# Performance work log

Measured on AMD Instinct MI355X. Metric: run time of the kernel, lower is better.

## Reference

```python
import jax, jax.numpy as jnp
import numpy as np
import math

B, SQ, SK = 8, 1024, 1024
DIM_Q = DIM_K = DIM_V = 512
H = 8
EPS = 1e-5
INF = jnp.float32(1e38)


def _ln(x, g, b):
    mu = jnp.mean(x, axis=-1, keepdims=True)
    var = jnp.mean(jnp.square(x - mu), axis=-1, keepdims=True)
    return (x - mu) * jax.lax.rsqrt(var + EPS) * g + b


def setup_inputs() -> dict:
    key = jax.random.key(0)
    ks = jax.random.split(key, 12)
    s = 1.0 / math.sqrt(DIM_V)
    return {
        "queries": jax.random.normal(ks[0], (B, SQ, DIM_Q), jnp.float32),
        "keys": jax.random.normal(ks[1], (B, SK, DIM_K), jnp.float32),
        # binary presence masks (as in the original usage)
        "presence_q": (jax.random.uniform(ks[2], (B, SQ)) > 0.1).astype(jnp.float32),
        "presence_k": (jax.random.uniform(ks[3], (B, SK)) > 0.1).astype(jnp.float32),
        "num_heads": H,
        "Wq": jax.random.normal(ks[4], (DIM_Q, DIM_V), jnp.float32) * s,
        "bq": jnp.zeros((DIM_V,), jnp.float32),
        "Wk": jax.random.normal(ks[5], (DIM_K, DIM_V), jnp.float32) * s,
        "bk": jnp.zeros((DIM_V,), jnp.float32),
        "Wv": jax.random.normal(ks[6], (DIM_K, DIM_V), jnp.float32) * s,
        "bv": jnp.zeros((DIM_V,), jnp.float32),
        "Wo": jax.random.normal(ks[7], (DIM_V, DIM_V), jnp.float32) * s,
        "bo": jnp.zeros((DIM_V,), jnp.float32),
        "g0": jnp.ones((DIM_V,), jnp.float32),
        "b0": jnp.zeros((DIM_V,), jnp.float32),
        "g1": jnp.ones((DIM_V,), jnp.float32),
        "b1": jnp.zeros((DIM_V,), jnp.float32),
    }


def reference(queries, keys, presence_q, presence_k, num_heads,
              Wq, bq, Wk, bk, Wv, bv, Wo, bo, g0, b0, g1, b1):
    b, sq, _ = queries.shape
    dim_v = Wq.shape[1]
    d = dim_v // num_heads
    q = queries @ Wq + bq                              # [B,Sq,V]
    k = keys @ Wk + bk                                 # [B,Sk,V]
    v = keys @ Wv + bv                                 # [B,Sk,V]
    qh = q.reshape(b, sq, num_heads, d)
    kh = k.reshape(b, -1, num_heads, d)
    vh = v.reshape(b, -1, num_heads, d)
    logits = jnp.einsum('bqhd,bkhd->bhqk', qh, kh) / jnp.float32(math.sqrt(dim_v))
    pq = presence_q[:, None, :, None]                  # [B,1,Sq,1]
    logits = pq * logits - (1.0 - pq) * INF
    pk = presence_k[:, None, None, :]                  # [B,1,1,Sk]
    logits = pk * logits - (1.0 - pk) * INF
    A = jax.nn.softmax(logits, axis=-1)                # [B,H,Sq,Sk]
    o = qh + jnp.einsum('bhqk,bkhd->bqhd', A, vh)      # residual add of Q_
    o = o.reshape(b, sq, dim_v)
    o = _ln(o, g0, b0)
    o = o + jax.nn.relu(o @ Wo + bo)
    o = _ln(o, g1, b1)
    return o
```

## Files before the change

### kernel.cpp

```cpp
#include <hip/hip_runtime.h>

typedef __attribute__((ext_vector_type(8))) short short8;
typedef __attribute__((ext_vector_type(4))) float f32x4;

#define SCALE2 0.06375871571f

__device__ __forceinline__ float bfu(unsigned short u){
  return __uint_as_float(((unsigned int)u) << 16);
}
__device__ __forceinline__ unsigned short f2b(float x){
  unsigned int b = __float_as_uint(x);
  return (unsigned short)((b + 0x7fffu + ((b>>16)&1u)) >> 16);
}
__device__ __forceinline__ uint4 pack8(const float* f){
  float4 a = *(const float4*)f, b = *(const float4*)(f+4);
  uint4 r;
  r.x = (unsigned)f2b(a.x) | ((unsigned)f2b(a.y)<<16);
  r.y = (unsigned)f2b(a.z) | ((unsigned)f2b(a.w)<<16);
  r.z = (unsigned)f2b(b.x) | ((unsigned)f2b(b.y)<<16);
  r.w = (unsigned)f2b(b.z) | ((unsigned)f2b(b.w)<<16);
  return r;
}

__global__ __launch_bounds__(256) void prep_inputs(
    const float* Wq, const float* Wk, const float* Wv, const float* Wo,
    const float* q, const float* k, unsigned short* wt, unsigned short* qk_dst)
{
  const int id = blockIdx.x, t = threadIdx.x;
  if (id < 256){
    const int m = id >> 6;
    const float* W = (m==0)?Wq:(m==1)?Wk:(m==2)?Wv:Wo;
    unsigned short* dst = wt + (long)m*262144;
    __shared__ unsigned short tile[64][72];
    const int n0 = ((id>>3)&7)*64, k0 = (id&7)*64;
    {
      int r = t>>2, c0 = (t&3)*16;
      uint4 u0 = pack8(W + (long)(k0+r)*512 + n0 + c0);
      uint4 u1 = pack8(W + (long)(k0+r)*512 + n0 + c0 + 8);
      unsigned short* us0 = (unsigned short*)&u0;
      unsigned short* us1 = (unsigned short*)&u1;
      #pragma unroll
      for (int i=0;i<8;++i) tile[c0+i][r] = us0[i];
      #pragma unroll
      for (int i=0;i<8;++i) tile[c0+8+i][r] = us1[i];
    }
    __syncthreads();
    {
      int n = t>>2, ks = (t&3)*16;
      *(uint4*)(dst + (long)(n0+n)*512 + k0 + ks)     = *(uint4*)&tile[n][ks];
      *(uint4*)(dst + (long)(n0+n)*512 + k0 + ks + 8) = *(uint4*)&tile[n][ks+8];
    }
  } else {
    long i = ((long)(id-256)*256 + t)*8;
    const float* src = (i < 4194304) ? q + i : k + (i - 4194304);
    *(uint4*)(qk_dst + i) = pack8(src);
  }
}

__global__ __launch_bounds__(256) void proj_mfma(
    const unsigned short* qin, const unsigned short* kin, const unsigned short* wt,
    const float* bq, const float* bk, const float* bv,
    unsigned short* q_bf, unsigned short* k_bf, unsigned short* vt_bf)
{
  const int mat = blockIdx.z;
  const unsigned short* A = (mat==0)? qin : kin;
  const unsigned short* Wt = wt + (long)mat*262144;
  const float* bias = (mat==0)?bq:(mat==1)?bk:bv;
  const int row0 = blockIdx.y*128, col0 = blockIdx.x*128;
  __shared__ unsigned short As[2][128][40];
  __shared__ unsigned short Ws[2][128][40];
  const int t = threadIdx.x;
  const int lane = t & 63, wid = t >> 6;
  const int ln = lane & 15, quad = lane >> 4;
  const int wy = wid >> 1, wx = wid & 1;
  f32x4 acc[4][4];
  #pragma unroll
  for (int i=0;i<4;++i){
    #pragma unroll
    for (int j=0;j<4;++j) acc[i][j] = (f32x4){0.f,0.f,0.f,0.f};
  }
  const int sr = t>>1, sk0 = (t&1)*16;
  const unsigned short* Arow = A  + (long)(row0+sr)*512 + sk0;
  const unsigned short* Wrow = Wt + (long)(col0+sr)*512 + sk0;
  uint4 a0 = *(const uint4*)(Arow);
  uint4 a1 = *(const uint4*)(Arow + 8);
  uint4 w0 = *(const uint4*)(Wrow);
  uint4 w1 = *(const uint4*)(Wrow + 8);
  *(uint4*)&As[0][sr][sk0]   = a0;
  *(uint4*)&As[0][sr][sk0+8] = a1;
  *(uint4*)&Ws[0][sr][sk0]   = w0;
  *(uint4*)&Ws[0][sr][sk0+8] = w1;
  __syncthreads();
  for (int it=0; it<16; ++it){
    const int cur = it & 1;
    if (it < 15){
      a0 = *(const uint4*)(Arow + (it+1)*32);
      a1 = *(const uint4*)(Arow + (it+1)*32 + 8);
      w0 = *(const uint4*)(Wrow + (it+1)*32);
      w1 = *(const uint4*)(Wrow + (it+1)*32 + 8);
    }
    short8 a[4], b[4];
    #pragma unroll
    for (int mt=0;mt<4;++mt) a[mt] = *(const short8*)&As[cur][wy*64+mt*16+ln][quad*8];
    #pragma unroll
    for (int nt=0;nt<4;++nt) b[nt] = *(const short8*)&Ws[cur][wx*64+nt*16+ln][quad*8];
    #pragma unroll
    for (int mt=0;mt<4;++mt){
      #pragma unroll
      for (int nt=0;nt<4;++nt)
        acc[mt][nt] = __builtin_amdgcn_mfma_f32_16x16x32_bf16(a[mt], b[nt], acc[mt][nt], 0,0,0);
    }
    if (it < 15){
      *(uint4*)&As[cur^1][sr][sk0]   = a0;
      *(uint4*)&As[cur^1][sr][sk0+8] = a1;
      *(uint4*)&Ws[cur^1][sr][sk0]   = w0;
      *(uint4*)&Ws[cur^1][sr][sk0+8] = w1;
    }
    __syncthreads();
  }
  float bias_v[4];
  #pragma unroll
  for (int nt=0;nt<4;++nt) bias_v[nt] = bias[col0 + wx*64 + nt*16 + ln];
  if (mat < 2){
    unsigned short* dst = (mat==0)? q_bf : k_bf;
    #pragma unroll
    for (int mt=0;mt<4;++mt){
      int row = row0 + wy*64 + mt*16 + quad*4;
      #pragma unroll
      for (int nt=0;nt<4;++nt){
        int col = col0 + wx*64 + nt*16 + ln;
        #pragma unroll
        for (int r=0;r<4;++r)
          dst[(long)(row+r)*512 + col] = f2b(acc[mt][nt][r] + bias_v[nt]);
      }
    }
  } else {
    #pragma unroll
    for (int mt=0;mt<4;++mt){
      int row = row0 + wy*64 + mt*16 + quad*4;
      int bb = row >> 10, sk = row & 1023;
      #pragma unroll
      for (int nt=0;nt<4;++nt){
        int col = col0 + wx*64 + nt*16 + ln;
        int h = col >> 6, dd = col & 63;
        uint2 pk2; unsigned short* pp = (unsigned short*)&pk2;
        #pragma unroll
        for (int r=0;r<4;++r) pp[r] = f2b(acc[mt][nt][r] + bias_v[nt]);
        *(uint2*)(vt_bf + (((long)((bb*8+h)*64+dd)) << 10) + sk) = pk2;
      }
    }
  }
}

__global__ __launch_bounds__(256, 2) void attn_mfma(
    const unsigned short* q_bf, const unsigned short* k_bf, const unsigned short* vt_bf,
    const float* pres_q, const float* pres_k, unsigned short* o_bf)
{
  const int bx = blockIdx.x;
  const int b = bx >> 3, h = bx & 7;
  const int q0 = blockIdx.y * 128;
  const int t = threadIdx.x;
  const int lane = t & 63, wid = t >> 6, ln = lane & 15, quad = lane >> 4;
  __shared__ unsigned short Pw[4][32][72];

  const unsigned short* Kb  = k_bf  + ((long)b*1024)*512 + h*64;
  const unsigned short* Vb  = vt_bf + (((long)(b*8+h)) << 16);
  const float* pkb = pres_k + b*1024;

  short8 aq[2][2];
  float av[2], mval[2];
  #pragma unroll
  for (int st=0;st<2;++st){
    int qi = q0 + wid*32 + st*16 + ln;
    const unsigned short* qrow = q_bf + ((long)(b*1024 + qi))*512 + h*64;
    aq[st][0] = *(const short8*)(qrow + quad*8);
    aq[st][1] = *(const short8*)(qrow + 32 + quad*8);
    av[st]   = SCALE2 * pres_q[b*1024 + qi];
    mval[st] = (av[st] == 0.f) ? 0.f : -43.f;
  }
  f32x4 oacc[2][4];
  #pragma unroll
  for (int st=0;st<2;++st){
    #pragma unroll
    for (int i=0;i<4;++i) oacc[st][i] = (f32x4){0.f,0.f,0.f,0.f};
  }
  float lsum[2] = {0.f, 0.f};

  short8 kf0[4], kf1[4];
  #pragma unroll
  for (int kt=0;kt<4;++kt){
    const unsigned short* kp = Kb + ((long)(kt*16+ln))*512 + quad*8;
    kf0[kt] = *(const short8*)kp;
    kf1[kt] = *(const short8*)(kp+32);
  }

  for (int it=0; it<16; ++it){
    const int k0 = it*64;
    short8 vf0[4], vf1[4];
    #pragma unroll
    for (int dt=0;dt<4;++dt){
      const unsigned short* vp = Vb + (((long)(dt*16+ln)) << 10) + k0 + quad*8;
      vf0[dt] = *(const short8*)vp;
      vf1[dt] = *(const short8*)(vp+32);
    }
    float4 pk4[4];
    #pragma unroll
    for (int kt=0;kt<4;++kt)
      pk4[kt] = *(const float4*)(pkb + k0 + kt*16 + quad*4);
    short8 nk0[4], nk1[4];
    if (it < 15){
      #pragma unroll
      for (int kt=0;kt<4;++kt){
        const unsigned short* kp = Kb + ((long)(k0+64+kt*16+ln))*512 + quad*8;
        nk0[kt] = *(const short8*)kp;
        nk1[kt] = *(const short8*)(kp+32);
      }
    }
    #pragma unroll
    for (int st=0;st<2;++st){
      f32x4 sc[4];
      #pragma unroll
      for (int kt=0;kt<4;++kt) sc[kt] = (f32x4){0.f,0.f,0.f,0.f};
      __builtin_amdgcn_s_setprio(1);
      #pragma unroll
      for (int kt=0;kt<4;++kt){
        sc[kt] = __builtin_amdgcn_mfma_f32_16x16x32_bf16(kf0[kt], aq[st][0], sc[kt], 0,0,0);
        sc[kt] = __builtin_amdgcn_mfma_f32_16x16x32_bf16(kf1[kt], aq[st][1], sc[kt], 0,0,0);
      }
      __builtin_amdgcn_s_setprio(0);
      #pragma unroll
      for (int kt=0;kt<4;++kt){
        float x0 = __builtin_fmaf(pk4[kt].x, __builtin_fmaf(sc[kt][0], av[st], -mval[st]), mval[st]);
        float x1 = __builtin_fmaf(pk4[kt].y, __builtin_fmaf(sc[kt][1], av[st], -mval[st]), mval[st]);
        float x2 = __builtin_fmaf(pk4[kt].z, __builtin_fmaf(sc[kt][2], av[st], -mval[st]), mval[st]);
        float x3 = __builtin_fmaf(pk4[kt].w, __builtin_fmaf(sc[kt][3], av[st], -mval[st]), mval[st]);
        float e0 = __builtin_amdgcn_exp2f(x0);
        float e1 = __builtin_amdgcn_exp2f(x1);
        float e2 = __builtin_amdgcn_exp2f(x2);
        float e3 = __builtin_amdgcn_exp2f(x3);
        lsum[st] += (e0+e1)+(e2+e3);
        uint2 w;
        w.x = (unsigned)f2b(e0) | ((unsigned)f2b(e1)<<16);
        w.y = (unsigned)f2b(e2) | ((unsigned)f2b(e3)<<16);
        *(uint2*)&Pw[wid][st*16+ln][kt*16 + quad*4] = w;
      }
    }
    #pragma unroll
    for (int st=0;st<2;++st){
      short8 ap0 = *(const short8*)&Pw[wid][st*16+ln][quad*8];
      short8 ap1 = *(const short8*)&Pw[wid][st*16+ln][32 + quad*8];
      __builtin_amdgcn_s_setprio(1);
      #pragma unroll
      for (int dt=0;dt<4;++dt){
        oacc[st][dt] = __builtin_amdgcn_mfma_f32_16x16x32_bf16(ap0, vf0[dt], oacc[st][dt], 0,0,0);
        oacc[st][dt] = __builtin_amdgcn_mfma_f32_16x16x32_bf16(ap1, vf1[dt], oacc[st][dt], 0,0,0);
      }
      __builtin_amdgcn_s_setprio(0);
    }
    if (it < 15){
      #pragma unroll
      for (int kt=0;kt<4;++kt){ kf0[kt] = nk0[kt]; kf1[kt] = nk1[kt]; }
    }
  }
  #pragma unroll
  for (int st=0;st<2;++st){
    float l = lsum[st];
    l += __shfl_xor(l, 16);
    l += __shfl_xor(l, 32);
    #pragma unroll
    for (int r=0;r<4;++r){
      float lr = __shfl(l, quad*4 + r);
      float inv = 1.f / lr;
      int ql = q0 + wid*32 + st*16 + quad*4 + r;
      long base = ((long)(b*1024 + ql))*512 + h*64;
      #pragma unroll
      for (int dt=0;dt<4;++dt){
        float qh = bfu(q_bf[base + dt*16 + ln]);
        o_bf[base + dt*16 + ln] = f2b(qh + oacc[st][dt][r]*inv);
      }
    }
  }
}

__global__ __launch_bounds__(256) void ln_kernel(
    const unsigned short* in, void* outp, int mode, const float* g, const float* bvec)
{
  const int row = blockIdx.x*4 + (threadIdx.x >> 6);
  const int lane = threadIdx.x & 63;
  uint4 raw = *(const uint4*)(in + (long)row*512 + lane*8);
  const unsigned short* rs16 = (const unsigned short*)&raw;
  float v[8];
  #pragma unroll
  for (int c=0;c<8;++c) v[c] = bfu(rs16[c]);
  float sum = 0.f;
  #pragma unroll
  for (int c=0;c<8;++c) sum += v[c];
  #pragma unroll
  for (int msk=1; msk<64; msk<<=1) sum += __shfl_xor(sum, msk);
  float mu = sum * (1.f/512.f);
  float var = 0.f;
  #pragma unroll
  for (int c=0;c<8;++c){ v[c] -= mu; var += v[c]*v[c]; }
  #pragma unroll
  for (int msk=1; msk<64; msk<<=1) var += __shfl_xor(var, msk);
  float rs = rsqrtf(var*(1.f/512.f) + 1e-5f);
  float gv[8], bv[8];
  *(float4*)&gv[0] = *(const float4*)(g + lane*8);
  *(float4*)&gv[4] = *(const float4*)(g + lane*8 + 4);
  *(float4*)&bv[0] = *(const float4*)(bvec + lane*8);
  *(float4*)&bv[4] = *(const float4*)(bvec + lane*8 + 4);
  float y[8];
  #pragma unroll
  for (int c=0;c<8;++c) y[c] = v[c]*rs*gv[c] + bv[c];
  if (mode){
    float* dst = (float*)outp + (long)row*512 + lane*8;
    *(float4*)dst       = *(float4*)&y[0];
    *(float4*)(dst + 4) = *(float4*)&y[4];
  } else {
    uint4 out; unsigned short* os = (unsigned short*)&out;
    #pragma unroll
    for (int c=0;c<8;++c) os[c] = f2b(y[c]);
    *(uint4*)((unsigned short*)outp + (long)row*512 + lane*8) = out;
  }
}

__global__ __launch_bounds__(256) void out_mfma(
    const unsigned short* t_bf, const unsigned short* Wt, const float* bo,
    unsigned short* u_bf)
{
  const int row0 = blockIdx.y*64, col0 = blockIdx.x*128;
  __shared__ unsigned short As[2][64][40];
  __shared__ unsigned short Ws[2][128][40];
  const int t = threadIdx.x;
  const int lane = t & 63, wid = t >> 6;
  const int ln = lane & 15, quad = lane >> 4;
  const int wy = wid >> 1, wx = wid & 1;
  f32x4 acc[2][4];
  #pragma unroll
  for (int i=0;i<2;++i){
    #pragma unroll
    for (int j=0;j<4;++j) acc[i][j] = (f32x4){0.f,0.f,0.f,0.f};
  }
  const int ar = t>>2, ac0 = (t&3)*8;
  const int wr = t>>1, wc0 = (t&1)*16;
  const unsigned short* Arow = t_bf + (long)(row0+ar)*512 + ac0;
  const unsigned short* Wrow = Wt   + (long)(col0+wr)*512 + wc0;
  uint4 a0 = *(const uint4*)(Arow);
  uint4 w0 = *(const uint4*)(Wrow);
  uint4 w1 = *(const uint4*)(Wrow + 8);
  *(uint4*)&As[0][ar][ac0] = a0;
  *(uint4*)&Ws[0][wr][wc0]   = w0;
  *(uint4*)&Ws[0][wr][wc0+8] = w1;
  __syncthreads();
  for (int it=0; it<16; ++it){
    const int cur = it & 1;
    if (it < 15){
      a0 = *(const uint4*)(Arow + (it+1)*32);
      w0 = *(const uint4*)(Wrow + (it+1)*32);
      w1 = *(const uint4*)(Wrow + (it+1)*32 + 8);
    }
    short8 a[2], b[4];
    #pragma unroll
    for (int mt=0;mt<2;++mt) a[mt] = *(const short8*)&As[cur][wy*32+mt*16+ln][quad*8];
    #pragma unroll
    for (int nt=0;nt<4;++nt) b[nt] = *(const short8*)&Ws[cur][wx*64+nt*16+ln][quad*8];
    #pragma unroll
    for (int mt=0;mt<2;++mt){
      #pragma unroll
      for (int nt=0;nt<4;++nt)
        acc[mt][nt] = __builtin_amdgcn_mfma_f32_16x16x32_bf16(a[mt], b[nt], acc[mt][nt], 0,0,0);
    }
    if (it < 15){
      *(uint4*)&As[cur^1][ar][ac0] = a0;
      *(uint4*)&Ws[cur^1][wr][wc0]   = w0;
      *(uint4*)&Ws[cur^1][wr][wc0+8] = w1;
    }
    __syncthreads();
  }
  float bias_v[4];
  #pragma unroll
  for (int nt=0;nt<4;++nt) bias_v[nt] = bo[col0 + wx*64 + nt*16 + ln];
  #pragma unroll
  for (int mt=0;mt<2;++mt){
    int row = row0 + wy*32 + mt*16 + quad*4;
    #pragma unroll
    for (int nt=0;nt<4;++nt){
      int col = col0 + wx*64 + nt*16 + ln;
      #pragma unroll
      for (int r=0;r<4;++r){
        long idx = (long)(row+r)*512 + col;
        float u = acc[mt][nt][r] + bias_v[nt];
        u = fmaxf(u, 0.f);
        u_bf[idx] = f2b(bfu(t_bf[idx]) + u);
      }
    }
  }
}

extern "C" void kernel_launch(void* const* d_in, const int* in_sizes, int n_in,
                              void* d_out, int out_size, void* d_ws, size_t ws_size,
                              hipStream_t stream)
{
  unsigned short* q_bf  = (unsigned short*)d_ws;
  unsigned short* k_bf  = q_bf  + 8192l*512;
  unsigned short* vt_bf = k_bf  + 8192l*512;
  unsigned short* t_bf  = vt_bf + 8192l*512;
  unsigned short* wt    = t_bf  + 8192l*512;
  unsigned short* qin   = wt + 4l*512*512;
  unsigned short* kin   = qin + 4194304;
  unsigned short* o_bf  = qin;
  unsigned short* u_bf  = kin;

  hipLaunchKernelGGL(prep_inputs, dim3(4352), dim3(256), 0, stream,
                     (const float*)d_in[5], (const float*)d_in[7],
                     (const float*)d_in[9], (const float*)d_in[11],
                     (const float*)d_in[0], (const float*)d_in[1], wt, qin);
  hipLaunchKernelGGL(proj_mfma, dim3(4,64,3), dim3(256), 0, stream,
                     qin, kin, wt,
                     (const float*)d_in[6], (const float*)d_in[8],
                     (const float*)d_in[10], q_bf, k_bf, vt_bf);
  hipLaunchKernelGGL(attn_mfma, dim3(64,8), dim3(256), 0, stream,
                     q_bf, k_bf, vt_bf,
                     (const float*)d_in[2], (const float*)d_in[3], o_bf);
  hipLaunchKernelGGL(ln_kernel, dim3(2048), dim3(256), 0, stream,
                     o_bf, (void*)t_bf, 0, (const float*)d_in[13], (const float*)d_in[14]);
  hipLaunchKernelGGL(out_mfma, dim3(4,128), dim3(256), 0, stream,
                     t_bf, wt + 3l*512*512, (const float*)d_in[12], u_bf);
  hipLaunchKernelGGL(ln_kernel, dim3(2048), dim3(256), 0, stream,
                     u_bf, d_out, 1, (const float*)d_in[15], (const float*)d_in[16]);
}
```

Before: 242.1 us.

## Stage K/V tiles in LDS and split keys across wave pairs in attention

The attention kernel now uses 512 threads per block and stages each 128-key K and V^T tile, plus key presence, in shared memory, so the block's waves share one tile instead of each loading K/V from global memory into registers. Waves are paired: each pair covers the same 32 queries and splits the key tile in halves. The partial outputs and row sums are merged through LDS at the end. Loads for the next tile are prefetched into registers while the current one is computed. This cuts redundant global traffic and register pressure, at the cost of two block barriers per tile, LDS read traffic, and an extra reduction step.

Result: faster. 222.3 us (-8.2%).

```diff
diff --git a/kernel.cpp b/kernel.cpp
--- a/kernel.cpp
+++ b/kernel.cpp
@@ -152,7 +152,7 @@
   }
 }
 
-__global__ __launch_bounds__(256, 2) void attn_mfma(
+__global__ __launch_bounds__(512, 4) void attn_mfma(
     const unsigned short* q_bf, const unsigned short* k_bf, const unsigned short* vt_bf,
     const float* pres_q, const float* pres_k, unsigned short* o_bf)
 {
@@ -161,17 +161,36 @@
   const int q0 = blockIdx.y * 128;
   const int t = threadIdx.x;
   const int lane = t & 63, wid = t >> 6, ln = lane & 15, quad = lane >> 4;
-  __shared__ unsigned short Pw[4][32][72];
-
-  const unsigned short* Kb  = k_bf  + ((long)b*1024)*512 + h*64;
-  const unsigned short* Vb  = vt_bf + (((long)(b*8+h)) << 16);
-  const float* pkb = pres_k + b*1024;
-
-  short8 aq[2][2];
-  float av[2], mval[2];
+  const int g = wid >> 1, khalf = wid & 1;
+
+  __shared__ unsigned short Ks[128][72];
+  __shared__ unsigned short Vt[64][136];
+  __shared__ unsigned short Pw[8][16][72];
+  __shared__ float pk_s[128];
+
+  const unsigned short* Kg = k_bf  + ((long)b*1024)*512 + h*64;
+  const unsigned short* Vg = vt_bf + (((long)(b*8+h)) << 16);
+  const float* pkg = pres_k + b*1024;
+
+  const int krow = t >> 2, kcol = (t & 3) * 16;
+  const int vrow = t >> 3, vcol = (t & 7) * 16;
+
+  {
+    uint4 ka = *(const uint4*)(Kg + (long)krow*512 + kcol);
+    uint4 kb = *(const uint4*)(Kg + (long)krow*512 + kcol + 8);
+    uint4 va = *(const uint4*)(Vg + (long)vrow*1024 + vcol);
+    uint4 vb = *(const uint4*)(Vg + (long)vrow*1024 + vcol + 8);
+    *(uint4*)&Ks[krow][kcol]   = ka;
+    *(uint4*)&Ks[krow][kcol+8] = kb;
+    *(uint4*)&Vt[vrow][vcol]   = va;
+    *(uint4*)&Vt[vrow][vcol+8] = vb;
+    if (t < 128) pk_s[t] = pkg[t];
+  }
+
+  short8 aq[2][2]; float av[2], mval[2];
   #pragma unroll
   for (int st=0;st<2;++st){
-    int qi = q0 + wid*32 + st*16 + ln;
+    int qi = q0 + g*32 + st*16 + ln;
     const unsigned short* qrow = q_bf + ((long)(b*1024 + qi))*512 + h*64;
     aq[st][0] = *(const short8*)(qrow + quad*8);
     aq[st][1] = *(const short8*)(qrow + 32 + quad*8);
@@ -185,55 +204,40 @@
     for (int i=0;i<4;++i) oacc[st][i] = (f32x4){0.f,0.f,0.f,0.f};
   }
   float lsum[2] = {0.f, 0.f};
-
-  short8 kf0[4], kf1[4];
-  #pragma unroll
-  for (int kt=0;kt<4;++kt){
-    const unsigned short* kp = Kb + ((long)(kt*16+ln))*512 + quad*8;
-    kf0[kt] = *(const short8*)kp;
-    kf1[kt] = *(const short8*)(kp+32);
-  }
-
-  for (int it=0; it<16; ++it){
-    const int k0 = it*64;
-    short8 vf0[4], vf1[4];
-    #pragma unroll
-    for (int dt=0;dt<4;++dt){
-      const unsigned short* vp = Vb + (((long)(dt*16+ln)) << 10) + k0 + quad*8;
-      vf0[dt] = *(const short8*)vp;
-      vf1[dt] = *(const short8*)(vp+32);
-    }
-    float4 pk4[4];
-    #pragma unroll
-    for (int kt=0;kt<4;++kt)
-      pk4[kt] = *(const float4*)(pkb + k0 + kt*16 + quad*4);
-    short8 nk0[4], nk1[4];
-    if (it < 15){
-      #pragma unroll
-      for (int kt=0;kt<4;++kt){
-        const unsigned short* kp = Kb + ((long)(k0+64+kt*16+ln))*512 + quad*8;
-        nk0[kt] = *(const short8*)kp;
-        nk1[kt] = *(const short8*)(kp+32);
-      }
-    }
-    #pragma unroll
-    for (int st=0;st<2;++st){
+  __syncthreads();
+
+  const int tb = khalf * 64;
+  for (int s=0; s<8; ++s){
+    uint4 pka, pkb, pva, pvb; float ppk = 0.f;
+    if (s < 7){
+      const long off = (long)(s+1)*128;
+      pka = *(const uint4*)(Kg + (off + krow)*512 + kcol);
+      pkb = *(const uint4*)(Kg + (off + krow)*512 + kcol + 8);
+      pva = *(const uint4*)(Vg + (long)vrow*1024 + off + vcol);
+      pvb = *(const uint4*)(Vg + (long)vrow*1024 + off + vcol + 8);
+      if (t < 128) ppk = pkg[off + t];
+    }
+    #pragma unroll
+    for (int st=0; st<2; ++st){
       f32x4 sc[4];
       #pragma unroll
       for (int kt=0;kt<4;++kt) sc[kt] = (f32x4){0.f,0.f,0.f,0.f};
       __builtin_amdgcn_s_setprio(1);
       #pragma unroll
       for (int kt=0;kt<4;++kt){
-        sc[kt] = __builtin_amdgcn_mfma_f32_16x16x32_bf16(kf0[kt], aq[st][0], sc[kt], 0,0,0);
-        sc[kt] = __builtin_amdgcn_mfma_f32_16x16x32_bf16(kf1[kt], aq[st][1], sc[kt], 0,0,0);
+        short8 kb0 = *(const short8*)&Ks[tb + kt*16+ln][quad*8];
+        short8 kb1 = *(const short8*)&Ks[tb + kt*16+ln][32+quad*8];
+        sc[kt] = __builtin_amdgcn_mfma_f32_16x16x32_bf16(kb0, aq[st][0], sc[kt], 0,0,0);
+        sc[kt] = __builtin_amdgcn_mfma_f32_16x16x32_bf16(kb1, aq[st][1], sc[kt], 0,0,0);
       }
       __builtin_amdgcn_s_setprio(0);
       #pragma unroll
       for (int kt=0;kt<4;++kt){
-        float x0 = __builtin_fmaf(pk4[kt].x, __builtin_fmaf(sc[kt][0], av[st], -mval[st]), mval[st]);
-        float x1 = __builtin_fmaf(pk4[kt].y, __builtin_fmaf(sc[kt][1], av[st], -mval[st]), mval[st]);
-        float x2 = __builtin_fmaf(pk4[kt].z, __builtin_fmaf(sc[kt][2], av[st], -mval[st]), mval[st]);
-        float x3 = __builtin_fmaf(pk4[kt].w, __builtin_fmaf(sc[kt][3], av[st], -mval[st]), mval[st]);
+        float4 pk4 = *(const float4*)&pk_s[tb + kt*16 + quad*4];
+        float x0 = __builtin_fmaf(pk4.x, __builtin_fmaf(sc[kt][0], av[st], -mval[st]), mval[st]);
+        float x1 = __builtin_fmaf(pk4.y, __builtin_fmaf(sc[kt][1], av[st], -mval[st]), mval[st]);
+        float x2 = __builtin_fmaf(pk4.z, __builtin_fmaf(sc[kt][2], av[st], -mval[st]), mval[st]);
+        float x3 = __builtin_fmaf(pk4.w, __builtin_fmaf(sc[kt][3], av[st], -mval[st]), mval[st]);
         float e0 = __builtin_amdgcn_exp2f(x0);
         float e1 = __builtin_amdgcn_exp2f(x1);
         float e2 = __builtin_amdgcn_exp2f(x2);
@@ -242,41 +246,66 @@
         uint2 w;
         w.x = (unsigned)f2b(e0) | ((unsigned)f2b(e1)<<16);
         w.y = (unsigned)f2b(e2) | ((unsigned)f2b(e3)<<16);
-        *(uint2*)&Pw[wid][st*16+ln][kt*16 + quad*4] = w;
-      }
-    }
-    #pragma unroll
-    for (int st=0;st<2;++st){
-      short8 ap0 = *(const short8*)&Pw[wid][st*16+ln][quad*8];
-      short8 ap1 = *(const short8*)&Pw[wid][st*16+ln][32 + quad*8];
+        *(uint2*)&Pw[wid][ln][kt*16 + quad*4] = w;
+      }
+      short8 ap0 = *(const short8*)&Pw[wid][ln][quad*8];
+      short8 ap1 = *(const short8*)&Pw[wid][ln][32 + quad*8];
       __builtin_amdgcn_s_setprio(1);
       #pragma unroll
       for (int dt=0;dt<4;++dt){
-        oacc[st][dt] = __builtin_amdgcn_mfma_f32_16x16x32_bf16(ap0, vf0[dt], oacc[st][dt], 0,0,0);
-        oacc[st][dt] = __builtin_amdgcn_mfma_f32_16x16x32_bf16(ap1, vf1[dt], oacc[st][dt], 0,0,0);
+        short8 vb0 = *(const short8*)&Vt[dt*16+ln][tb + quad*8];
+        short8 vb1 = *(const short8*)&Vt[dt*16+ln][tb + 32 + quad*8];
+        oacc[st][dt] = __builtin_amdgcn_mfma_f32_16x16x32_bf16(ap0, vb0, oacc[st][dt], 0,0,0);
+        oacc[st][dt] = __builtin_amdgcn_mfma_f32_16x16x32_bf16(ap1, vb1, oacc[st][dt], 0,0,0);
       }
       __builtin_amdgcn_s_setprio(0);
     }
-    if (it < 15){
-      #pragma unroll
-      for (int kt=0;kt<4;++kt){ kf0[kt] = nk0[kt]; kf1[kt] = nk1[kt]; }
-    }
-  }
-  #pragma unroll
-  for (int st=0;st<2;++st){
-    float l = lsum[st];
-    l += __shfl_xor(l, 16);
-    l += __shfl_xor(l, 32);
-    #pragma unroll
-    for (int r=0;r<4;++r){
-      float lr = __shfl(l, quad*4 + r);
-      float inv = 1.f / lr;
-      int ql = q0 + wid*32 + st*16 + quad*4 + r;
-      long base = ((long)(b*1024 + ql))*512 + h*64;
+    __syncthreads();
+    if (s < 7){
+      *(uint4*)&Ks[krow][kcol]   = pka;
+      *(uint4*)&Ks[krow][kcol+8] = pkb;
+      *(uint4*)&Vt[vrow][vcol]   = pva;
+      *(uint4*)&Vt[vrow][vcol+8] = pvb;
+      if (t < 128) pk_s[t] = ppk;
+      __syncthreads();
+    }
+  }
+
+  float* MSf = (float*)&Pw[0][0][0];
+  #pragma unroll
+  for (int st=0; st<2; ++st){
+    __syncthreads();
+    if (khalf == 1){
+      float* m = MSf + (g*64 + lane)*18;
       #pragma unroll
       for (int dt=0;dt<4;++dt){
-        float qh = bfu(q_bf[base + dt*16 + ln]);
-        o_bf[base + dt*16 + ln] = f2b(qh + oacc[st][dt][r]*inv);
+        #pragma unroll
+        for (int r=0;r<4;++r) m[dt*4+r] = oacc[st][dt][r];
+      }
+      m[16] = lsum[st];
+    }
+    __syncthreads();
+    if (khalf == 0){
+      const float* m = MSf + (g*64 + lane)*18;
+      float l = lsum[st] + m[16];
+      #pragma unroll
+      for (int dt=0;dt<4;++dt){
+        #pragma unroll
+        for (int r=0;r<4;++r) oacc[st][dt][r] += m[dt*4+r];
+      }
+      l += __shfl_xor(l, 16);
+      l += __shfl_xor(l, 32);
+      #pragma unroll
+      for (int r=0;r<4;++r){
+        float lr = __shfl(l, quad*4 + r);
+        float inv = 1.f / lr;
+        int ql = q0 + g*32 + st*16 + quad*4 + r;
+        long base = ((long)(b*1024 + ql))*512 + h*64;
+        #pragma unroll
+        for (int dt=0;dt<4;++dt){
+          float qh = bfu(q_bf[base + dt*16 + ln]);
+          o_bf[base + dt*16 + ln] = f2b(qh + oacc[st][dt][r]*inv);
+        }
       }
     }
   }
@@ -419,7 +448,7 @@
                      qin, kin, wt,
                      (const float*)d_in[6], (const float*)d_in[8],
                      (const float*)d_in[10], q_bf, k_bf, vt_bf);
-  hipLaunchKernelGGL(attn_mfma, dim3(64,8), dim3(256), 0, stream,
+  hipLaunchKernelGGL(attn_mfma, dim3(64,8), dim3(512), 0, stream,
                      q_bf, k_bf, vt_bf,
                      (const float*)d_in[2], (const float*)d_in[3], o_bf);
   hipLaunchKernelGGL(ln_kernel, dim3(2048), dim3(256), 0, stream,
```
